# Kernel optimization log

Measured on AMD Instinct MI355X. Metric: run time of the kernel, lower is better.

The kernel has to match this reference:

```python
import jax, jax.numpy as jnp
import numpy as np

# Static hyperparams matching init_kwargs
KSIZE, STRIDE, PAD, DIL = 3, 2, 1, 1


def setup_inputs() -> dict:
    key = jax.random.key(0)
    k1, k2 = jax.random.split(key)
    B, H, W, Cin, Cout = 8, 128, 128, 128, 256
    feats = jax.random.normal(k1, (B * H * W, Cin), dtype=jnp.float32)
    weight = jax.random.normal(k2, (KSIZE * KSIZE, Cin, Cout), dtype=jnp.float32) * 0.05
    alpha_upper = jnp.ones((1,), dtype=jnp.float32)
    # dense grid coords [N, 3] = (batch, y, x), matching a dense image sparse tensor
    bb, yy, xx = np.meshgrid(np.arange(B), np.arange(H), np.arange(W), indexing='ij')
    coords = jnp.asarray(np.stack([bb, yy, xx], -1).reshape(-1, 3), dtype=jnp.int32)
    return {"feats": feats, "weight": weight, "alpha_upper": alpha_upper,
            "coords": coords, "H": H, "W": W, "B": B}


def _coord_ranges(H, W):
    # Faithful translation of WrappedMinkowskiStridedOperation.__init__ + forward
    # coordinate math, specialized to a dense grid (per-batch min=0, max=H-1/W-1).
    kernel_origin = DIL * ((KSIZE - 1) // 2) * (KSIZE % 2)
    dilated = DIL * (KSIZE - 1) + 1
    ks_off = kernel_origin - dilated + 1          # _kernel_start_offset
    ke_off = kernel_origin                        # _kernel_end_offset
    idx_start = kernel_origin - PAD               # _index_start_offset
    ranges = []
    for ext in (H, W):
        idx_end = (ext - 1) + kernel_origin + PAD - dilated + 2
        start = max(idx_start, (0 + ks_off - idx_start) // STRIDE * STRIDE + idx_start)
        end = min(idx_end, ((ext - 1 + ke_off - idx_start) // STRIDE + 1) * STRIDE + idx_start)
        ranges.append(np.arange(start, end, STRIDE))
    offsets = np.arange(KSIZE) * DIL - kernel_origin  # kernel region offsets
    return ranges[0], ranges[1], offsets, idx_start


def reference(feats, weight, alpha_upper, coords, H, W, B):
    Cin = feats.shape[1]
    Cout = weight.shape[-1]
    ys, xs, offs, idx_start = _coord_ranges(H, W)
    OH, OW = len(ys), len(xs)
    oy, ox = jnp.meshgrid(jnp.asarray(ys, jnp.int32), jnp.asarray(xs, jnp.int32), indexing='ij')
    dy, dx = np.meshgrid(offs, offs, indexing='ij')
    dy = jnp.asarray(dy.reshape(-1), jnp.int32)  # [kvol]
    dx = jnp.asarray(dx.reshape(-1), jnp.int32)
    ny = oy[None] + dy[:, None, None]            # [kvol, OH, OW]
    nx = ox[None] + dx[:, None, None]
    valid = (ny >= 0) & (ny < H) & (nx >= 0) & (nx < W)
    lin = jnp.clip(ny, 0, H - 1) * W + jnp.clip(nx, 0, W - 1)  # [kvol, OH, OW]
    feats3 = feats.reshape(B, H * W, Cin)
    gathered = feats3[:, lin]                    # [B, kvol, OH, OW, Cin]
    gathered = jnp.where(valid[None, ..., None], gathered, jnp.zeros((), feats.dtype))
    out = jnp.einsum('bkhwc,kcd->bhwd', gathered, weight)  # [B, OH, OW, Cout]
    out_feats = out.reshape(B * OH * OW, Cout)
    # output coordinates, remapped as in forward (shift by index_start, divide by stride)
    oc = jnp.stack([oy, ox], -1).reshape(-1, 2)  # [OH*OW, 2]
    oc = (oc - jnp.int32(idx_start)) // jnp.int32(STRIDE)
    oc = jnp.tile(oc, (B, 1))
    bcol = jnp.repeat(jnp.arange(B, dtype=jnp.int32), OH * OW)
    out_coords = jnp.concatenate([bcol[:, None], oc], axis=1)
    return out_feats, out_coords, alpha_upper
```

## Files before the change

kernel.cpp:

```cpp
#include <hip/hip_runtime.h>


#define OUT_FEATS_ELEMS (32768 * 256)
#define OUT_COORDS_OFF  OUT_FEATS_ELEMS
#define ALPHA_OFF       (OUT_FEATS_ELEMS + 32768 * 3)

typedef float v16f __attribute__((ext_vector_type(16)));

__device__ __forceinline__ unsigned pk4fp8(float a, float b, float c, float d) {
    unsigned u = 0;
    u = __builtin_amdgcn_cvt_pk_fp8_f32(a, b, u, false);
    u = __builtin_amdgcn_cvt_pk_fp8_f32(c, d, u, true);
    return u;
}

#define GLOAD_LDS16(SRC, DST)                                                  \
    __builtin_amdgcn_global_load_lds(                                          \
        (const __attribute__((address_space(1))) void*)(SRC),                  \
        (__attribute__((address_space(3))) void*)(DST), 16, 0, 0)

__global__ void feats8_kernel(const float4* __restrict__ f, uint2* __restrict__ o) {
    int i = blockIdx.x * 256 + threadIdx.x;
    float4 a = f[2 * i];
    float4 b = f[2 * i + 1];
    uint2 r;
    r.x = pk4fp8(a.x, a.y, a.z, a.w);
    r.y = pk4fp8(b.x, b.y, b.z, b.w);
    o[i] = r;
}

__global__ void wt_coords_kernel(const float* __restrict__ w, unsigned char* __restrict__ Bw,
                                 float* __restrict__ out, const float* __restrict__ alpha) {
    int cid = blockIdx.x * 256 + threadIdx.x;
    if (cid < 32768) {
        int b = cid >> 12, iy = (cid >> 6) & 63, ix = cid & 63;
        float* c = out + OUT_COORDS_OFF + (size_t)cid * 3;
        c[0] = (float)b; c[1] = (float)iy; c[2] = (float)ix;
        if (cid == 0) out[ALPHA_OFF] = alpha[0];
    }
    if (cid < 18432) {
        int ch  = cid & 7;
        int row = (cid >> 3) & 127;
        int t   = cid >> 10;
        int nb  = (t >= 9) ? 1 : 0;
        int tap = t - 9 * nb;
        int chp = ch ^ (row & 7);
        int n   = (nb << 7) + row;
        int kb  = (tap << 7) + (chp << 4);
        unsigned u[4];
#pragma unroll
        for (int q = 0; q < 4; ++q) {
            float f0 = w[(size_t)(kb + 4 * q + 0) * 256 + n];
            float f1 = w[(size_t)(kb + 4 * q + 1) * 256 + n];
            float f2 = w[(size_t)(kb + 4 * q + 2) * 256 + n];
            float f3 = w[(size_t)(kb + 4 * q + 3) * 256 + n];
            u[q] = pk4fp8(f0, f1, f2, f3);
        }
        uint4 r; r.x = u[0]; r.y = u[1]; r.z = u[2]; r.w = u[3];
        *(uint4*)(Bw + (size_t)cid * 16) = r;
    }
}

__global__ void coords_alpha_kernel(float* __restrict__ out, const float* __restrict__ alpha) {
    int i = blockIdx.x * 256 + threadIdx.x;
    int b = i >> 12, iy = (i >> 6) & 63, ix = i & 63;
    float* c = out + OUT_COORDS_OFF + (size_t)i * 3;
    c[0] = (float)b; c[1] = (float)iy; c[2] = (float)ix;
    if (i == 0) out[ALPHA_OFF] = alpha[0];
}

__global__ __launch_bounds__(256, 2) void gemm_conv_kernel(
    const unsigned char* __restrict__ F8,
    const unsigned char* __restrict__ Bw,
    float* __restrict__ out)
{
    __shared__ unsigned char At[128 * 128];
    __shared__ unsigned char Bs[128 * 128];

    const int tid  = threadIdx.x;
    const int bid  = blockIdx.x;
    const int my   = bid & 255;
    const int nb   = bid >> 8;
    const int n0   = nb << 7;
    const int m0   = my << 7;
    const int bb   = my >> 5;
    const int iy0  = (my << 1) & 63;

    const int lane = tid & 63, wave = tid >> 6;
    const int wm   = (wave >> 1) << 6;
    const int wn   = (wave & 1) << 6;
    const int l31  = lane & 31;
    const int hh   = lane >> 5;
    const int xorl = l31 & 7;

    const int srow = lane >> 3;
    const int chp  = (lane & 7) ^ srow;
    const long rowA0 = (long)bb << 14;
    const unsigned char* bimg = Bw + ((size_t)(nb * 9) << 14) + ((size_t)wave << 12) + ((size_t)lane << 4);
    unsigned char* adst0 = At + (wave << 12);
    unsigned char* bdst0 = Bs + (wave << 12);

    v16f acc[2][2];
#pragma unroll
    for (int i = 0; i < 2; i++)
#pragma unroll
        for (int j = 0; j < 2; j++) acc[i][j] = (v16f)(0.0f);

    for (int tap = 0; tap < 9; ++tap) {
        const int dy = tap / 3 - 1;
        const int dx = tap % 3 - 1;

        __syncthreads();
#pragma unroll
        for (int it = 0; it < 4; ++it) {
            const int region = (wave << 2) + it;
            GLOAD_LDS16(bimg + ((size_t)tap << 14) + (it << 10), bdst0 + (it << 10));
            const int row = (region << 3) + srow;
            const int iyl = row >> 6, ix = row & 63;
            const int ny  = ((iy0 + iyl) << 1) + dy;
            const int nx  = (ix << 1) + dx;
            if (((unsigned)ny < 128u) & ((unsigned)nx < 128u)) {
                const unsigned char* asrc =
                    F8 + ((rowA0 + ((long)ny << 7) + nx) << 7) + (chp << 4);
                GLOAD_LDS16(asrc, adst0 + (it << 10));
            } else {
                uint4 z; z.x = 0u; z.y = 0u; z.z = 0u; z.w = 0u;
                *(uint4*)(At + (region << 10) + (lane << 4)) = z;
            }
        }
        __syncthreads();

#pragma unroll
        for (int seg = 0; seg < 8; ++seg) {
            const int q = seg ^ xorl;
            long long a[2], b[2];
#pragma unroll
            for (int i = 0; i < 2; i++)
                a[i] = *(const long long*)(At + ((wm + (i << 5) + l31) << 7) + (q << 4) + (hh << 3));
#pragma unroll
            for (int j = 0; j < 2; j++)
                b[j] = *(const long long*)(Bs + ((wn + (j << 5) + l31) << 7) + (q << 4) + (hh << 3));
#pragma unroll
            for (int i = 0; i < 2; i++)
#pragma unroll
                for (int j = 0; j < 2; j++)
                    acc[i][j] = __builtin_amdgcn_mfma_f32_32x32x16_fp8_fp8(a[i], b[j], acc[i][j], 0, 0, 0);
        }
    }

#pragma unroll
    for (int i = 0; i < 2; i++)
#pragma unroll
        for (int j = 0; j < 2; j++) {
            const int gcol = n0 + wn + (j << 5) + l31;
#pragma unroll
            for (int r = 0; r < 16; ++r) {
                const int grow = m0 + wm + (i << 5) + (r & 3) + ((r >> 2) << 3) + (hh << 2);
                out[(size_t)grow * 256 + gcol] = acc[i][j][r];
            }
        }
}

__global__ void naive_conv_kernel(const float* __restrict__ feats,
                                  const float* __restrict__ w,
                                  float* __restrict__ out) {
    int m = blockIdx.x;
    int n = threadIdx.x;
    int bb = m >> 12, iy = (m >> 6) & 63, ix = m & 63;
    float acc = 0.f;
    for (int tap = 0; tap < 9; ++tap) {
        int ny = 2 * iy + tap / 3 - 1;
        int nx = 2 * ix + tap % 3 - 1;
        if ((unsigned)ny < 128u && (unsigned)nx < 128u) {
            const float* fr = feats + ((size_t)((bb << 14) + (ny << 7) + nx) << 7);
            const float* wr = w + tap * 32768 + n;
            for (int c = 0; c < 128; ++c) acc += fr[c] * wr[c * 256];
        }
    }
    out[(size_t)m * 256 + n] = acc;
}

extern "C" void kernel_launch(void* const* d_in, const int* in_sizes, int n_in,
                              void* d_out, int out_size, void* d_ws, size_t ws_size,
                              hipStream_t stream) {
    const float* feats  = (const float*)d_in[0];
    const float* weight = (const float*)d_in[1];
    const float* alpha  = (const float*)d_in[2];
    float* out = (float*)d_out;

    const size_t NEED = (size_t)16777216 + (size_t)18 * 16384;
    if (ws_size >= NEED) {
        unsigned char* F8 = (unsigned char*)d_ws;
        unsigned char* Bw = F8 + 16777216;
        feats8_kernel<<<8192, 256, 0, stream>>>((const float4*)feats, (uint2*)F8);
        wt_coords_kernel<<<144, 256, 0, stream>>>(weight, Bw, out, alpha);
        gemm_conv_kernel<<<512, 256, 0, stream>>>(F8, Bw, out);
    } else {
        coords_alpha_kernel<<<128, 256, 0, stream>>>(out, alpha);
        naive_conv_kernel<<<32768, 256, 0, stream>>>(feats, weight, out);
    }
}
```

Measured before the change: 136.0 us.

## Double-buffer LDS tiles across taps and merge prep kernels into one launch

The GEMM kernel now keeps two LDS buffers for the A and B tiles. It issues the global-to-LDS loads for the next tap before running the MFMAs on the current tap, hiding load latency behind compute. The fp8 feature conversion and the weight/coords prep kernels are merged into a single launch to save one kernel launch. The cost is doubled LDS use per block, which may limit occupancy, plus reliance on correct wait insertion for the async LDS loads.

```diff
diff --git a/kernel.cpp b/kernel.cpp
--- a/kernel.cpp
+++ b/kernel.cpp
@@ -19,19 +19,23 @@
         (const __attribute__((address_space(1))) void*)(SRC),                  \
         (__attribute__((address_space(3))) void*)(DST), 16, 0, 0)
 
-__global__ void feats8_kernel(const float4* __restrict__ f, uint2* __restrict__ o) {
-    int i = blockIdx.x * 256 + threadIdx.x;
-    float4 a = f[2 * i];
-    float4 b = f[2 * i + 1];
-    uint2 r;
-    r.x = pk4fp8(a.x, a.y, a.z, a.w);
-    r.y = pk4fp8(b.x, b.y, b.z, b.w);
-    o[i] = r;
-}
-
-__global__ void wt_coords_kernel(const float* __restrict__ w, unsigned char* __restrict__ Bw,
-                                 float* __restrict__ out, const float* __restrict__ alpha) {
-    int cid = blockIdx.x * 256 + threadIdx.x;
+__global__ void prep_kernel(const float* __restrict__ feats, const float* __restrict__ w,
+                            const float* __restrict__ alpha,
+                            unsigned char* __restrict__ F8, unsigned char* __restrict__ Bw,
+                            float* __restrict__ out) {
+    int bid = blockIdx.x;
+    if (bid < 8192) {
+        int i = bid * 256 + threadIdx.x;
+        const float4* f = (const float4*)feats;
+        float4 a = f[2 * i];
+        float4 b = f[2 * i + 1];
+        uint2 r;
+        r.x = pk4fp8(a.x, a.y, a.z, a.w);
+        r.y = pk4fp8(b.x, b.y, b.z, b.w);
+        ((uint2*)F8)[i] = r;
+        return;
+    }
+    int cid = (bid - 8192) * 256 + threadIdx.x;
     if (cid < 32768) {
         int b = cid >> 12, iy = (cid >> 6) & 63, ix = cid & 63;
         float* c = out + OUT_COORDS_OFF + (size_t)cid * 3;
@@ -74,8 +78,8 @@
     const unsigned char* __restrict__ Bw,
     float* __restrict__ out)
 {
-    __shared__ unsigned char At[128 * 128];
-    __shared__ unsigned char Bs[128 * 128];
+    __shared__ unsigned char At[2][128 * 128];
+    __shared__ unsigned char Bs[2][128 * 128];
 
     const int tid  = threadIdx.x;
     const int bid  = blockIdx.x;
@@ -97,8 +101,6 @@
     const int chp  = (lane & 7) ^ srow;
     const long rowA0 = (long)bb << 14;
     const unsigned char* bimg = Bw + ((size_t)(nb * 9) << 14) + ((size_t)wave << 12) + ((size_t)lane << 4);
-    unsigned char* adst0 = At + (wave << 12);
-    unsigned char* bdst0 = Bs + (wave << 12);
 
     v16f acc[2][2];
 #pragma unroll
@@ -106,11 +108,11 @@
 #pragma unroll
         for (int j = 0; j < 2; j++) acc[i][j] = (v16f)(0.0f);
 
-    for (int tap = 0; tap < 9; ++tap) {
+    auto stage = [&](int tap, int b) {
         const int dy = tap / 3 - 1;
         const int dx = tap % 3 - 1;
-
-        __syncthreads();
+        unsigned char* adst0 = At[b] + (wave << 12);
+        unsigned char* bdst0 = Bs[b] + (wave << 12);
 #pragma unroll
         for (int it = 0; it < 4; ++it) {
             const int region = (wave << 2) + it;
@@ -125,26 +127,33 @@
                 GLOAD_LDS16(asrc, adst0 + (it << 10));
             } else {
                 uint4 z; z.x = 0u; z.y = 0u; z.z = 0u; z.w = 0u;
-                *(uint4*)(At + (region << 10) + (lane << 4)) = z;
+                *(uint4*)(At[b] + (region << 10) + (lane << 4)) = z;
             }
         }
+    };
+
+    stage(0, 0);
+
+    for (int tap = 0; tap < 9; ++tap) {
+        const int b = tap & 1;
         __syncthreads();
+        if (tap < 8) stage(tap + 1, b ^ 1);
 
 #pragma unroll
         for (int seg = 0; seg < 8; ++seg) {
             const int q = seg ^ xorl;
-            long long a[2], b[2];
+            long long a[2], bb2[2];
 #pragma unroll
             for (int i = 0; i < 2; i++)
-                a[i] = *(const long long*)(At + ((wm + (i << 5) + l31) << 7) + (q << 4) + (hh << 3));
+                a[i] = *(const long long*)(At[b] + ((wm + (i << 5) + l31) << 7) + (q << 4) + (hh << 3));
 #pragma unroll
             for (int j = 0; j < 2; j++)
-                b[j] = *(const long long*)(Bs + ((wn + (j << 5) + l31) << 7) + (q << 4) + (hh << 3));
+                bb2[j] = *(const long long*)(Bs[b] + ((wn + (j << 5) + l31) << 7) + (q << 4) + (hh << 3));
 #pragma unroll
             for (int i = 0; i < 2; i++)
 #pragma unroll
                 for (int j = 0; j < 2; j++)
-                    acc[i][j] = __builtin_amdgcn_mfma_f32_32x32x16_fp8_fp8(a[i], b[j], acc[i][j], 0, 0, 0);
+                    acc[i][j] = __builtin_amdgcn_mfma_f32_32x32x16_fp8_fp8(a[i], bb2[j], acc[i][j], 0, 0, 0);
         }
     }
 
@@ -192,8 +201,7 @@
     if (ws_size >= NEED) {
         unsigned char* F8 = (unsigned char*)d_ws;
         unsigned char* Bw = F8 + 16777216;
-        feats8_kernel<<<8192, 256, 0, stream>>>((const float4*)feats, (uint2*)F8);
-        wt_coords_kernel<<<144, 256, 0, stream>>>(weight, Bw, out, alpha);
+        prep_kernel<<<8336, 256, 0, stream>>>(feats, weight, alpha, F8, Bw, out);
         gemm_conv_kernel<<<512, 256, 0, stream>>>(F8, Bw, out);
     } else {
         coords_alpha_kernel<<<128, 256, 0, stream>>>(out, alpha);
```

Measured after the change: 133.8 us. No clear change (-1.6%).
